# Kernel tuning notes

Measured on AMD Instinct MI355X. Metric: run time of the kernel, lower is better.

## Reference

```python
import jax, jax.numpy as jnp
import numpy as np

HEADS = 16
DIM_HEAD = 128
SCALE = DIM_HEAD ** -0.5


def rotate_half(x):
    # x: (..., d) with d even; pairs (x1, x2) -> (-x2, x1)
    x = x.reshape(*x.shape[:-1], -1, 2)
    x1, x2 = x[..., 0], x[..., 1]
    return jnp.stack([-x2, x1], axis=-1).reshape(*x.shape[:-2], -1)


def apply_rotary(freqs, t):
    # freqs: (n, d), t: (b, h, n, d)
    cos = jnp.cos(freqs)[None, None]
    sin = jnp.sin(freqs)[None, None]
    return t * cos + rotate_half(t) * sin


def setup_inputs() -> dict:
    key = jax.random.key(0)
    ks = jax.random.split(key, 6)
    b, n, dim = 2, 2048, 2048
    inner = HEADS * DIM_HEAD
    s = dim ** -0.5
    x = jax.random.normal(ks[0], (b, n, dim), dtype=jnp.float32)
    rotary_emb = jax.random.normal(ks[1], (n, DIM_HEAD), dtype=jnp.float32)
    Wq = jax.random.normal(ks[2], (dim, inner), dtype=jnp.float32) * s
    Wkv = jax.random.normal(ks[3], (dim, 2 * inner), dtype=jnp.float32) * s
    Wo = jax.random.normal(ks[4], (inner, dim), dtype=jnp.float32) * s
    bo = jnp.zeros((dim,), dtype=jnp.float32)
    return {"x": x, "rotary_emb": rotary_emb, "Wq": Wq, "Wkv": Wkv, "Wo": Wo, "bo": bo}


def reference(x, rotary_emb, Wq, Wkv, Wo, bo):
    b, n, _ = x.shape
    q = x @ Wq                      # (b, n, inner)
    kv = x @ Wkv                    # (b, n, 2*inner)
    k, v = jnp.split(kv, 2, axis=-1)
    # b n (h d) -> b h n d
    split = lambda t: t.reshape(b, n, HEADS, DIM_HEAD).transpose(0, 2, 1, 3)
    q, k, v = split(q), split(k), split(v)
    q = apply_rotary(rotary_emb, q)
    k = apply_rotary(rotary_emb, k)
    q = q * SCALE
    dots = jnp.einsum('bhid,bhjd->bhij', q, k)
    attn = jax.nn.softmax(dots, axis=-1)
    out = jnp.einsum('bhij,bhjd->bhid', attn, v)
    out = out.transpose(0, 2, 1, 3).reshape(b, n, HEADS * DIM_HEAD)
    return out @ Wo + bo
```

## Files before the change

kernel.cpp:

```cpp
#include <hip/hip_runtime.h>
#include <stdint.h>

typedef __attribute__((ext_vector_type(8))) short s16x8;
typedef __attribute__((ext_vector_type(4))) float f32x4;

#define DEVFN static __device__ __forceinline__

constexpr int   S_LEN = 2048;
constexpr int   DH    = 128;
constexpr int   INNER = 2048;
constexpr float ASCALE = 0.08838834764831845f;

DEVFN float b2f(unsigned short u) {
  union { unsigned int i; float f; } v; v.i = ((unsigned int)u) << 16; return v.f;
}
DEVFN unsigned short f2b(float f) {
  union { float f; unsigned int i; } v; v.f = f;
  unsigned int r = v.i + 0x7fffu + ((v.i >> 16) & 1u);
  return (unsigned short)(r >> 16);
}
DEVFN void async_cp16(const unsigned short* g, unsigned short* l) {
  __builtin_amdgcn_global_load_lds((const __attribute__((address_space(1))) void*)g,
                                   (__attribute__((address_space(3))) void*)l, 16, 0, 0);
}

__global__ __launch_bounds__(256) void cvt_bf16_k(const float* __restrict__ in,
                                                  unsigned short* __restrict__ out) {
  const size_t e = ((size_t)blockIdx.x * 256 + threadIdx.x) * 8;
  const float4 a = *(const float4*)(in + e);
  const float4 b = *(const float4*)(in + e + 4);
  union { s16x8 v; unsigned short u[8]; } o;
  o.u[0] = f2b(a.x); o.u[1] = f2b(a.y); o.u[2] = f2b(a.z); o.u[3] = f2b(a.w);
  o.u[4] = f2b(b.x); o.u[5] = f2b(b.y); o.u[6] = f2b(b.z); o.u[7] = f2b(b.w);
  *(s16x8*)(out + e) = o.v;
}

__global__ __launch_bounds__(256) void rot_cs_k(const float* __restrict__ rot,
                                                float2* __restrict__ cst) {
  const int idx = blockIdx.x * 256 + threadIdx.x;
  const float f = rot[idx];
  float s, c;
  __sincosf(f, &s, &c);
  cst[idx] = make_float2(c, s);
}

__global__ __launch_bounds__(256) void transpose_cvt_k(const float* __restrict__ in,
                                                       unsigned short* __restrict__ out,
                                                       int R, int C) {
  __shared__ __align__(16) unsigned short tile[64][72];
  const int t  = threadIdx.x;
  const int lr = t >> 3;
  const int lc = (t & 7) << 3;
  const size_t ibase = (size_t)blockIdx.y * 64 * C + (size_t)blockIdx.x * 64;
#pragma unroll
  for (int rr = 0; rr < 64; rr += 32) {
    const float* p = in + ibase + (size_t)(rr + lr) * C + lc;
    const float4 a = *(const float4*)p;
    const float4 b = *(const float4*)(p + 4);
    unsigned short* tp = &tile[rr + lr][lc];
    tp[0] = f2b(a.x); tp[1] = f2b(a.y); tp[2] = f2b(a.z); tp[3] = f2b(a.w);
    tp[4] = f2b(b.x); tp[5] = f2b(b.y); tp[6] = f2b(b.z); tp[7] = f2b(b.w);
  }
  __syncthreads();
  const size_t obase = (size_t)blockIdx.x * 64 * R + (size_t)blockIdx.y * 64;
#pragma unroll
  for (int rr = 0; rr < 64; rr += 32) {
    int oc = rr + lr;
    union { s16x8 v; unsigned short s[8]; } u;
#pragma unroll
    for (int j = 0; j < 8; ++j) u.s[j] = tile[lc + j][oc];
    *(s16x8*)(out + obase + (size_t)oc * R + lc) = u.v;
  }
}

template <int EPI>
__global__ __launch_bounds__(256) void gemm_bt(
    const unsigned short* __restrict__ A,
    const unsigned short* __restrict__ Bt,
    unsigned short* __restrict__ out0,
    unsigned short* __restrict__ out1,
    unsigned short* __restrict__ out2,
    float* __restrict__ outf,
    const float* __restrict__ biasf,
    const float2* __restrict__ rotcs,
    int M, int N, int K) {
  __shared__ __align__(16) unsigned short smem[16384];
  unsigned short* As = smem;
  unsigned short* Bs = smem + 8192;
  const int tid  = threadIdx.x;
  const int wave = tid >> 6, lane = tid & 63;
  const int wm = wave & 1, wn = wave >> 1;
  const int quad = lane >> 4, l15 = lane & 15;
  const int l7 = l15 & 7;
  const int m0 = blockIdx.x * 128, n0 = blockIdx.y * 128;

  f32x4 acc[4][4];
#pragma unroll
  for (int i = 0; i < 4; ++i)
#pragma unroll
    for (int j = 0; j < 4; ++j) acc[i][j] = {0.f, 0.f, 0.f, 0.f};

  const int lrow = lane >> 3;
  const int lchk = (lane & 7) ^ (lrow & 7);
  const unsigned short* a_g = A  + (size_t)(m0 + wave * 32 + lrow) * K + (lchk << 3);
  const unsigned short* b_g = Bt + (size_t)(n0 + wave * 32 + lrow) * K + (lchk << 3);
  unsigned short* As_w = As + (wave * 32) * 64;
  unsigned short* Bs_w = Bs + (wave * 32) * 64;

  for (int k0 = 0; k0 < K; k0 += 64) {
    __syncthreads();
#pragma unroll
    for (int t = 0; t < 4; ++t) {
      async_cp16(a_g + k0 + (size_t)(t * 8) * K, As_w + t * 8 * 64);
      async_cp16(b_g + k0 + (size_t)(t * 8) * K, Bs_w + t * 8 * 64);
    }
    __syncthreads();
#pragma unroll
    for (int ks = 0; ks < 2; ++ks) {
      s16x8 af[4], bfr[4];
#pragma unroll
      for (int mi = 0; mi < 4; ++mi)
        af[mi] = *(const s16x8*)(As + (wm * 64 + mi * 16 + l15) * 64 + (((ks * 4 + quad) ^ l7) << 3));
#pragma unroll
      for (int ni = 0; ni < 4; ++ni)
        bfr[ni] = *(const s16x8*)(Bs + (wn * 64 + ni * 16 + l15) * 64 + (((ks * 4 + quad) ^ l7) << 3));
#pragma unroll
      for (int mi = 0; mi < 4; ++mi)
#pragma unroll
        for (int ni = 0; ni < 4; ++ni)
          acc[mi][ni] = __builtin_amdgcn_mfma_f32_16x16x32_bf16(af[mi], bfr[ni], acc[mi][ni], 0, 0, 0);
    }
  }

  if constexpr (EPI == 1) {
#pragma unroll
    for (int mi = 0; mi < 4; ++mi)
#pragma unroll
      for (int ni = 0; ni < 4; ++ni)
#pragma unroll
        for (int r = 0; r < 4; ++r) {
          const int gm = m0 + wm * 64 + mi * 16 + quad * 4 + r;
          const int gn = n0 + wn * 64 + ni * 16 + l15;
          outf[(size_t)gm * N + gn] = acc[mi][ni][r] + biasf[gn];
        }
  } else {
    __syncthreads();
    const int b     = m0 >> 11;
    const int ibase = m0 & 2047;
    if (n0 < 2 * INNER) {
      const bool isq = (n0 < INNER);
      const int h = (n0 & (INNER - 1)) >> 7;
#pragma unroll
      for (int mi = 0; mi < 4; ++mi)
#pragma unroll
        for (int ni = 0; ni < 4; ++ni) {
          const int dd = wn * 64 + ni * 16 + l15;
          const int ch = dd >> 3;
#pragma unroll
          for (int r = 0; r < 4; ++r) {
            const int il = wm * 64 + mi * 16 + quad * 4 + r;
            const float v  = acc[mi][ni][r];
            const float vp = __shfl_xor(v, 1);
            const float2 cs = rotcs[(size_t)(ibase + il) * 128 + dd];
            float rv = (dd & 1) ? fmaf(v, cs.x,  vp * cs.y)
                                : fmaf(v, cs.x, -vp * cs.y);
            if (isq) rv *= ASCALE;
            smem[il * 128 + ((ch ^ (il & 7)) << 3) + (dd & 7)] = f2b(rv);
          }
        }
      __syncthreads();
      unsigned short* outp = (isq ? out0 : out1) +
                             ((size_t)((b << 4) + h) * S_LEN + ibase) * DH;
#pragma unroll
      for (int it = 0; it < 8; ++it) {
        const int f  = it * 256 + tid;
        const int il = f >> 4, ch = f & 15;
        s16x8 vv = *(const s16x8*)(smem + il * 128 + ((ch ^ (il & 7)) << 3));
        *(s16x8*)(outp + (size_t)il * DH + (ch << 3)) = vv;
      }
    } else {
      const int h = (n0 - 2 * INNER) >> 7;
#pragma unroll
      for (int mi = 0; mi < 4; ++mi)
#pragma unroll
        for (int ni = 0; ni < 4; ++ni) {
          const int dd = wn * 64 + ni * 16 + l15;
#pragma unroll
          for (int r = 0; r < 4; ++r) {
            const int il = wm * 64 + mi * 16 + quad * 4 + r;
            smem[dd * 128 + (((il >> 3) ^ (dd & 7)) << 3) + (il & 7)] = f2b(acc[mi][ni][r]);
          }
        }
      __syncthreads();
      unsigned short* outp = out2 + (size_t)((b << 4) + h) * DH * S_LEN + ibase;
#pragma unroll
      for (int it = 0; it < 8; ++it) {
        const int f  = it * 256 + tid;
        const int dd = f >> 4, ch = f & 15;
        s16x8 vv = *(const s16x8*)(smem + dd * 128 + ((ch ^ (dd & 7)) << 3));
        *(s16x8*)(outp + (size_t)dd * S_LEN + (ch << 3)) = vv;
      }
    }
  }
}

__global__ __launch_bounds__(256, 2) void flash_attn(
    const unsigned short* __restrict__ q,
    const unsigned short* __restrict__ k,
    const unsigned short* __restrict__ vt,
    unsigned short* __restrict__ aout) {
  __shared__ __align__(16) unsigned short Ks[64 * 128];
  __shared__ __align__(16) unsigned short Vs[128 * 64];
  __shared__ __align__(16) unsigned short Ps[4][32 * 64];
  const int tid = threadIdx.x;
  const int w = tid >> 6, lane = tid & 63;
  const int quad = lane >> 4, l15 = lane & 15;
  const int l7 = l15 & 7;
  const int i0 = blockIdx.x * 128;
  const int bh = blockIdx.y;
  const unsigned short* qh = q  + (size_t)bh * S_LEN * DH;
  const unsigned short* kh = k  + (size_t)bh * S_LEN * DH;
  const unsigned short* vh = vt + (size_t)bh * DH * S_LEN;

  s16x8 qf[2][4];
#pragma unroll
  for (int mi = 0; mi < 2; ++mi)
#pragma unroll
    for (int ks = 0; ks < 4; ++ks)
      qf[mi][ks] = *(const s16x8*)(qh + (size_t)(i0 + w * 32 + mi * 16 + l15) * DH + ks * 32 + quad * 8);

  f32x4 oacc[2][8];
#pragma unroll
  for (int mi = 0; mi < 2; ++mi)
#pragma unroll
    for (int ni = 0; ni < 8; ++ni) oacc[mi][ni] = {0.f, 0.f, 0.f, 0.f};
  float mrun[2][4], lrun[2][4];
#pragma unroll
  for (int mi = 0; mi < 2; ++mi)
#pragma unroll
    for (int r = 0; r < 4; ++r) { mrun[mi][r] = -1e30f; lrun[mi][r] = 0.f; }

  unsigned short* Pw = Ps[w];

  for (int j0 = 0; j0 < S_LEN; j0 += 64) {
    __syncthreads();
#pragma unroll
    for (int v = 0; v < 4; ++v) {
      const int off = v * 2048 + tid * 8;
      const int kr = off >> 7, kc = off & 127;
      *(s16x8*)(Ks + kr * 128 + ((((kc >> 3) ^ (kr & 7))) << 3)) =
          *(const s16x8*)(kh + (size_t)(j0 + kr) * DH + kc);
      const int vr = off >> 6, vc = off & 63;
      *(s16x8*)(Vs + vr * 64 + ((((vc >> 3) ^ (vr & 7))) << 3)) =
          *(const s16x8*)(vh + (size_t)vr * S_LEN + j0 + vc);
    }
    __syncthreads();

    f32x4 sacc[2][4];
#pragma unroll
    for (int mi = 0; mi < 2; ++mi)
#pragma unroll
      for (int ni = 0; ni < 4; ++ni) sacc[mi][ni] = {0.f, 0.f, 0.f, 0.f};
#pragma unroll
    for (int ks = 0; ks < 4; ++ks) {
      s16x8 kb[4];
#pragma unroll
      for (int ni = 0; ni < 4; ++ni)
        kb[ni] = *(const s16x8*)(Ks + (ni * 16 + l15) * 128 + (((ks * 4 + quad) ^ l7) << 3));
#pragma unroll
      for (int mi = 0; mi < 2; ++mi)
#pragma unroll
        for (int ni = 0; ni < 4; ++ni)
          sacc[mi][ni] = __builtin_amdgcn_mfma_f32_16x16x32_bf16(qf[mi][ks], kb[ni], sacc[mi][ni], 0, 0, 0);
    }

#pragma unroll
    for (int mi = 0; mi < 2; ++mi)
#pragma unroll
      for (int r = 0; r < 4; ++r) {
        float v = fmaxf(fmaxf(sacc[mi][0][r], sacc[mi][1][r]),
                        fmaxf(sacc[mi][2][r], sacc[mi][3][r]));
        v = fmaxf(v, __shfl_xor(v, 1));
        v = fmaxf(v, __shfl_xor(v, 2));
        v = fmaxf(v, __shfl_xor(v, 4));
        v = fmaxf(v, __shfl_xor(v, 8));
        const float mnew  = fmaxf(mrun[mi][r], v);
        const float alpha = __expf(mrun[mi][r] - mnew);
        mrun[mi][r] = mnew;
        float s0 = 0.f;
#pragma unroll
        for (int ni = 0; ni < 4; ++ni) {
          float p = __expf(sacc[mi][ni][r] - mnew);
          sacc[mi][ni][r] = p;
          s0 += p;
        }
        s0 += __shfl_xor(s0, 1);
        s0 += __shfl_xor(s0, 2);
        s0 += __shfl_xor(s0, 4);
        s0 += __shfl_xor(s0, 8);
        lrun[mi][r] = lrun[mi][r] * alpha + s0;
#pragma unroll
        for (int ni = 0; ni < 8; ++ni) oacc[mi][ni][r] *= alpha;
      }

#pragma unroll
    for (int mi = 0; mi < 2; ++mi)
#pragma unroll
      for (int ni = 0; ni < 4; ++ni) {
        const int col = ni * 16 + l15;
        const int ch  = col >> 3;
#pragma unroll
        for (int r = 0; r < 4; ++r) {
          const int row = mi * 16 + quad * 4 + r;
          Pw[row * 64 + ((ch ^ (row & 7)) << 3) + (col & 7)] = f2b(sacc[mi][ni][r]);
        }
      }
    __threadfence_block();

#pragma unroll
    for (int ks = 0; ks < 2; ++ks) {
      const int swz = ((ks * 4 + quad) ^ l7) << 3;
      s16x8 pf[2];
#pragma unroll
      for (int mi = 0; mi < 2; ++mi)
        pf[mi] = *(const s16x8*)(Pw + (mi * 16 + l15) * 64 + swz);
#pragma unroll
      for (int ni = 0; ni < 8; ++ni) {
        s16x8 vb = *(const s16x8*)(Vs + (ni * 16 + l15) * 64 + swz);
#pragma unroll
        for (int mi = 0; mi < 2; ++mi)
          oacc[mi][ni] = __builtin_amdgcn_mfma_f32_16x16x32_bf16(pf[mi], vb, oacc[mi][ni], 0, 0, 0);
      }
    }
  }

  const int b = bh >> 4, h = bh & 15;
#pragma unroll
  for (int mi = 0; mi < 2; ++mi)
#pragma unroll
    for (int r = 0; r < 4; ++r) {
      const float inv = 1.0f / lrun[mi][r];
      const int i = i0 + w * 32 + mi * 16 + quad * 4 + r;
#pragma unroll
      for (int ni = 0; ni < 8; ++ni) {
        const int dd = ni * 16 + l15;
        aout[((size_t)b * S_LEN + i) * INNER + h * DH + dd] = f2b(oacc[mi][ni][r] * inv);
      }
    }
}

extern "C" void kernel_launch(void* const* d_in, const int* in_sizes, int n_in,
                              void* d_out, int out_size, void* d_ws, size_t ws_size,
                              hipStream_t stream) {
  const float* x   = (const float*)d_in[0];
  const float* rot = (const float*)d_in[1];
  const float* Wq  = (const float*)d_in[2];
  const float* Wkv = (const float*)d_in[3];
  const float* Wo  = (const float*)d_in[4];
  const float* bo  = (const float*)d_in[5];
  float* out = (float*)d_out;

  unsigned short* ws = (unsigned short*)d_ws;
  unsigned short* wt  = ws;
  unsigned short* wot = wt  + (size_t)6144 * 2048;
  unsigned short* qb  = wot + (size_t)2048 * 2048;
  unsigned short* kb  = qb  + (size_t)32 * 2048 * 128;
  unsigned short* vtb = kb  + (size_t)32 * 2048 * 128;
  unsigned short* xb  = vtb + (size_t)32 * 2048 * 128;
  unsigned short* att = wt;

  float2* cst = (float2*)d_out;

  rot_cs_k<<<dim3(1024), 256, 0, stream>>>(rot, cst);
  cvt_bf16_k<<<dim3(4096), 256, 0, stream>>>(x, xb);
  transpose_cvt_k<<<dim3(32, 32), 256, 0, stream>>>(Wq,  wt, 2048, 2048);
  transpose_cvt_k<<<dim3(64, 32), 256, 0, stream>>>(Wkv, wt + (size_t)2048 * 2048, 2048, 4096);
  transpose_cvt_k<<<dim3(32, 32), 256, 0, stream>>>(Wo,  wot, 2048, 2048);

  gemm_bt<0><<<dim3(32, 48), 256, 0, stream>>>(xb, wt, qb, kb, vtb, nullptr, nullptr, cst, 4096, 6144, 2048);
  flash_attn<<<dim3(16, 32), 256, 0, stream>>>(qb, kb, vtb, att);
  gemm_bt<1><<<dim3(32, 16), 256, 0, stream>>>(att, wot, nullptr, nullptr, nullptr, out, bo, nullptr, 4096, 2048, 2048);
}
```

Measured before the change: 471.0 us.

## Double-buffer K/V tiles with async LDS loads, lazy rescale, XCD-aware block mapping

Double-buffers the K/V shared-memory tiles and fills them with global_load_lds async copies one iteration ahead, so global loads overlap with the MFMA work. This removes one barrier per iteration. The online softmax now rescales only when the running max grows by more than a threshold (8), and skips the accumulator rescale when no lane in the wave needs it. The per-row sum reduction across lanes moves out of the loop to the epilogue. Block indices are remapped so that blocks sharing the same head land on the same XCD, which should improve L2 reuse of K/V. The cost is double the K/V LDS, which may lower occupancy, and the buffered K/V loads must be correctly complete before use, since only a barrier at the end of the iteration guards them.

```diff
diff --git a/kernel.cpp b/kernel.cpp
--- a/kernel.cpp
+++ b/kernel.cpp
@@ -204,20 +204,38 @@
   }
 }
 
+DEVFN void stage_tile(const unsigned short* kh, const unsigned short* vh,
+                      int j0, unsigned short* KsB, unsigned short* VsB, int tid) {
+#pragma unroll
+  for (int v = 0; v < 4; ++v) {
+    const int off = v * 2048 + tid * 8;
+    const int kr = off >> 7;
+    const int kc = (((off & 127) >> 3) ^ (kr & 7)) << 3;
+    async_cp16(kh + (size_t)(j0 + kr) * DH + kc, KsB + off);
+    const int vr = off >> 6;
+    const int vc = (((off & 63) >> 3) ^ (vr & 7)) << 3;
+    async_cp16(vh + (size_t)vr * S_LEN + j0 + vc, VsB + off);
+  }
+}
+
 __global__ __launch_bounds__(256, 2) void flash_attn(
     const unsigned short* __restrict__ q,
     const unsigned short* __restrict__ k,
     const unsigned short* __restrict__ vt,
     unsigned short* __restrict__ aout) {
-  __shared__ __align__(16) unsigned short Ks[64 * 128];
-  __shared__ __align__(16) unsigned short Vs[128 * 64];
+  __shared__ __align__(16) unsigned short Ks[2][64 * 128];
+  __shared__ __align__(16) unsigned short Vs[2][128 * 64];
   __shared__ __align__(16) unsigned short Ps[4][32 * 64];
   const int tid = threadIdx.x;
   const int w = tid >> 6, lane = tid & 63;
   const int quad = lane >> 4, l15 = lane & 15;
   const int l7 = l15 & 7;
-  const int i0 = blockIdx.x * 128;
-  const int bh = blockIdx.y;
+
+  const int lin  = blockIdx.y * 16 + blockIdx.x;
+  const int xcd  = lin & 7, slot = lin >> 3;
+  const int bh   = (xcd << 2) + (slot >> 4);
+  const int i0   = (slot & 15) * 128;
+
   const unsigned short* qh = q  + (size_t)bh * S_LEN * DH;
   const unsigned short* kh = k  + (size_t)bh * S_LEN * DH;
   const unsigned short* vh = vt + (size_t)bh * DH * S_LEN;
@@ -242,19 +260,15 @@
 
   unsigned short* Pw = Ps[w];
 
+  stage_tile(kh, vh, 0, Ks[0], Vs[0], tid);
+  __syncthreads();
+  int cur = 0;
+
   for (int j0 = 0; j0 < S_LEN; j0 += 64) {
-    __syncthreads();
-#pragma unroll
-    for (int v = 0; v < 4; ++v) {
-      const int off = v * 2048 + tid * 8;
-      const int kr = off >> 7, kc = off & 127;
-      *(s16x8*)(Ks + kr * 128 + ((((kc >> 3) ^ (kr & 7))) << 3)) =
-          *(const s16x8*)(kh + (size_t)(j0 + kr) * DH + kc);
-      const int vr = off >> 6, vc = off & 63;
-      *(s16x8*)(Vs + vr * 64 + ((((vc >> 3) ^ (vr & 7))) << 3)) =
-          *(const s16x8*)(vh + (size_t)vr * S_LEN + j0 + vc);
-    }
-    __syncthreads();
+    if (j0 + 64 < S_LEN)
+      stage_tile(kh, vh, j0 + 64, Ks[cur ^ 1], Vs[cur ^ 1], tid);
+    const unsigned short* Ksc = Ks[cur];
+    const unsigned short* Vsc = Vs[cur];
 
     f32x4 sacc[2][4];
 #pragma unroll
@@ -266,7 +280,7 @@
       s16x8 kb[4];
 #pragma unroll
       for (int ni = 0; ni < 4; ++ni)
-        kb[ni] = *(const s16x8*)(Ks + (ni * 16 + l15) * 128 + (((ks * 4 + quad) ^ l7) << 3));
+        kb[ni] = *(const s16x8*)(Ksc + (ni * 16 + l15) * 128 + (((ks * 4 + quad) ^ l7) << 3));
 #pragma unroll
       for (int mi = 0; mi < 2; ++mi)
 #pragma unroll
@@ -274,6 +288,8 @@
           sacc[mi][ni] = __builtin_amdgcn_mfma_f32_16x16x32_bf16(qf[mi][ks], kb[ni], sacc[mi][ni], 0, 0, 0);
     }
 
+    float al[2][4];
+    int anyresc = 0;
 #pragma unroll
     for (int mi = 0; mi < 2; ++mi)
 #pragma unroll
@@ -284,9 +300,13 @@
         v = fmaxf(v, __shfl_xor(v, 2));
         v = fmaxf(v, __shfl_xor(v, 4));
         v = fmaxf(v, __shfl_xor(v, 8));
-        const float mnew  = fmaxf(mrun[mi][r], v);
-        const float alpha = __expf(mrun[mi][r] - mnew);
+        const float mo   = mrun[mi][r];
+        const int   resc = v > mo + 8.f;
+        const float mnew = resc ? v : mo;
+        const float a    = resc ? __expf(mo - v) : 1.f;
         mrun[mi][r] = mnew;
+        al[mi][r]   = a;
+        anyresc |= resc;
         float s0 = 0.f;
 #pragma unroll
         for (int ni = 0; ni < 4; ++ni) {
@@ -294,14 +314,16 @@
           sacc[mi][ni][r] = p;
           s0 += p;
         }
-        s0 += __shfl_xor(s0, 1);
-        s0 += __shfl_xor(s0, 2);
-        s0 += __shfl_xor(s0, 4);
-        s0 += __shfl_xor(s0, 8);
-        lrun[mi][r] = lrun[mi][r] * alpha + s0;
-#pragma unroll
-        for (int ni = 0; ni < 8; ++ni) oacc[mi][ni][r] *= alpha;
-      }
+        lrun[mi][r] = lrun[mi][r] * a + s0;
+      }
+    if (__any(anyresc)) {
+#pragma unroll
+      for (int mi = 0; mi < 2; ++mi)
+#pragma unroll
+        for (int ni = 0; ni < 8; ++ni)
+#pragma unroll
+          for (int r = 0; r < 4; ++r) oacc[mi][ni][r] *= al[mi][r];
+    }
 
 #pragma unroll
     for (int mi = 0; mi < 2; ++mi)
@@ -326,12 +348,15 @@
         pf[mi] = *(const s16x8*)(Pw + (mi * 16 + l15) * 64 + swz);
 #pragma unroll
       for (int ni = 0; ni < 8; ++ni) {
-        s16x8 vb = *(const s16x8*)(Vs + (ni * 16 + l15) * 64 + swz);
+        s16x8 vb = *(const s16x8*)(Vsc + (ni * 16 + l15) * 64 + swz);
 #pragma unroll
         for (int mi = 0; mi < 2; ++mi)
           oacc[mi][ni] = __builtin_amdgcn_mfma_f32_16x16x32_bf16(pf[mi], vb, oacc[mi][ni], 0, 0, 0);
       }
     }
+
+    __syncthreads();
+    cur ^= 1;
   }
 
   const int b = bh >> 4, h = bh & 15;
@@ -339,7 +364,12 @@
   for (int mi = 0; mi < 2; ++mi)
 #pragma unroll
     for (int r = 0; r < 4; ++r) {
-      const float inv = 1.0f / lrun[mi][r];
+      float l = lrun[mi][r];
+      l += __shfl_xor(l, 1);
+      l += __shfl_xor(l, 2);
+      l += __shfl_xor(l, 4);
+      l += __shfl_xor(l, 8);
+      const float inv = 1.0f / l;
       const int i = i0 + w * 32 + mi * 16 + quad * 4 + r;
 #pragma unroll
       for (int ni = 0; ni < 8; ++ni) {
```

Result: faster. 438.1 us (-7.0%).
